# Kernel optimization log

Hardware: AMD Instinct MI355X
Metric: run time of the kernel (lower is better)

## Reference

```python
import jax, jax.numpy as jnp
import numpy as np
from math import ceil, log2

N_ROWS, M_COLS = 4096, 4096
LEVELS, FILT_LEN = 8, 16


def circ_conv(a, b, n):
    # circular convolution of each row of a with filter b, both zero-padded/truncated to length n
    return jnp.fft.irfft(jnp.fft.rfft(a, n=n) * jnp.fft.rfft(b, n=n), n=n)


def forward_level(x, w):
    # one forward DWT step over rows of x using wavelet filter w
    part = x.shape[1] // 2
    g = jnp.flip(w).at[1::2].multiply(-1.0)  # scaling filter g_k = (-1)^k h_{M-k-1}
    we, wo = w[::2], w[1::2]
    ge, go = g[::2], g[1::2]
    even, odd = x[:, ::2], x[:, 1::2]
    details = circ_conv(even, we, part) + circ_conv(odd, wo, part)
    approx = circ_conv(even, ge, part) + circ_conv(odd, go, part)
    return details, approx


def backward_level(details, approx, w):
    # one inverse DWT step: zero-upsample then circular-convolve with synthesis filters
    ws = jnp.flip(w)                       # wavelet synthesis
    ss = w.at[1::2].multiply(-1.0)         # scaling synthesis
    n, md = details.shape
    fd = jnp.zeros((n, 2 * md), details.dtype).at[:, ::2].set(details)
    fa = jnp.zeros((n, 2 * approx.shape[1]), approx.dtype).at[:, ::2].set(approx)
    return circ_conv(fd, ws, 2 * md) + circ_conv(fa, ss, 2 * approx.shape[1])


def despawn(x, wavelet):
    input_length = x.shape[1]
    target = 2 ** ceil(log2(input_length))
    x = jnp.pad(x, ((0, 0), (0, target - input_length)), mode='edge')  # ReplicationPad1d
    levels = wavelet.shape[0]
    approx = x
    coeffs = []
    for lvl in range(levels):
        d, approx = forward_level(approx, wavelet[lvl])
        coeffs.append(d)
    coeffs.append(approx)
    # inverse transform (note: original applies no thresholding in forward)
    rec = coeffs[-1]
    for lvl in reversed(range(levels)):
        rec = backward_level(coeffs[lvl], rec, wavelet[lvl])
    return rec[:, :input_length], jnp.concatenate(coeffs, axis=-1)


def setup_inputs() -> dict:
    key = jax.random.key(0)
    k1, k2 = jax.random.split(key)
    inp = jax.random.normal(k1, (N_ROWS, M_COLS), dtype=jnp.float32)
    wavelet = jax.random.normal(k2, (LEVELS, FILT_LEN), dtype=jnp.float32) * 0.3
    return {"input": inp, "wavelet": wavelet}


def reference(input, wavelet):
    return despawn(input, wavelet)
```

## Files before the change

kernel.cpp:

```cpp
#include <hip/hip_runtime.h>

#define NROWS 4096
#define NCOLS 4096
#define TPB   256

__global__ __launch_bounds__(TPB, 4) void despawn_kernel(
    const float* __restrict__ in, const float* __restrict__ wv,
    float* __restrict__ out_rec, float* __restrict__ out_coef)
{
    __shared__ float S[10240];
    float* C = S + 6144;
    const int row = blockIdx.x;
    const int tid = threadIdx.x;
    const float* rowIn = in + (size_t)row * NCOLS;

    {
        float* E = S;
        float* O = S + 2048;
        for (int i = tid; i < 1024; i += TPB) {
            float4 v = reinterpret_cast<const float4*>(rowIn)[i];
            *reinterpret_cast<float2*>(E + 2 * i) = make_float2(v.x, v.z);
            *reinterpret_cast<float2*>(O + 2 * i) = make_float2(v.y, v.w);
        }
    }
    __syncthreads();

    {
        float* E  = S;
        float* O  = S + 2048;
        float* E2 = S + 4096;
        float* O2 = S + 5120;
        int part = 2048;
        for (int lvl = 0; lvl < 8; ++lvl) {
            const float* w = wv + lvl * 16;
            float wl[16];
            #pragma unroll
            for (int q = 0; q < 16; ++q) wl[q] = w[q];
            float* det = C + (4096 - 2 * part);
            float* lastA = C + 4080;
            const bool last = (lvl == 7);
            const int pm = part - 1;
            for (int k = tid; k < part; k += TPB) {
                float d = 0.f, a = 0.f;
                #pragma unroll
                for (int t = 0; t < 8; ++t) {
                    int i = (k - t) & pm;
                    float xe = E[i], xo = O[i];
                    d = fmaf(wl[2 * t], xe, d);
                    d = fmaf(wl[2 * t + 1], xo, d);
                    a = fmaf(wl[15 - 2 * t], xe, a);
                    a = fmaf(-wl[14 - 2 * t], xo, a);
                }
                det[k] = d;
                if (last) {
                    lastA[k] = a;
                } else {
                    float* dst = (k & 1) ? O2 : E2;
                    dst[k >> 1] = a;
                }
            }
            __syncthreads();
            float* t0 = E; E = E2; E2 = t0;
            float* t1 = O; O = O2; O2 = t1;
            part >>= 1;
        }
    }

    {
        float* R0 = S;
        float* R1 = S + 4096;
        const float* A = C + 4080;
        int md = 16;
        for (int lvl = 7; lvl >= 0; --lvl) {
            const float* w = wv + lvl * 16;
            float wl[16];
            #pragma unroll
            for (int q = 0; q < 16; ++q) wl[q] = w[q];
            const float* D = C + (4096 - 2 * md);
            float* out = (lvl & 1) ? R1 : R0;
            const int mm = md - 1;
            for (int j = tid; j < md; j += TPB) {
                float r0 = 0.f, r1 = 0.f;
                #pragma unroll
                for (int t = 0; t < 8; ++t) {
                    int i = (j - t) & mm;
                    float dv = D[i], av = A[i];
                    r0 = fmaf(wl[15 - 2 * t], dv, r0);
                    r0 = fmaf(wl[2 * t],      av, r0);
                    r1 = fmaf(wl[14 - 2 * t], dv, r1);
                    r1 = fmaf(-wl[2 * t + 1], av, r1);
                }
                *reinterpret_cast<float2*>(out + 2 * j) = make_float2(r0, r1);
            }
            __syncthreads();
            A = out;
            md <<= 1;
        }
    }

    {
        const float* R0 = S;
        float* orow = out_rec  + (size_t)row * NCOLS;
        float* crow = out_coef + (size_t)row * NCOLS;
        for (int i = tid; i < 1024; i += TPB) {
            reinterpret_cast<float4*>(orow)[i] = reinterpret_cast<const float4*>(R0)[i];
            reinterpret_cast<float4*>(crow)[i] = reinterpret_cast<const float4*>(C)[i];
        }
    }
}

extern "C" void kernel_launch(void* const* d_in, const int* in_sizes, int n_in,
                              void* d_out, int out_size, void* d_ws, size_t ws_size,
                              hipStream_t stream) {
    (void)in_sizes; (void)n_in; (void)d_ws; (void)ws_size; (void)out_size;
    const float* in = (const float*)d_in[0];
    const float* wv = (const float*)d_in[1];
    float* out_rec  = (float*)d_out;
    float* out_coef = (float*)d_out + (size_t)NROWS * NCOLS;
    despawn_kernel<<<NROWS, TPB, 0, stream>>>(in, wv, out_rec, out_coef);
}
```

Before: 65.14 us.

## Register-block the large DWT levels with vectorized sliding-window LDS loads

The large forward and inverse levels now give each thread a contiguous run of 8, 4 or 2 outputs. Each thread loads a sliding window of inputs into registers with float4/float2 LDS reads, so the scalar reads of 8 taps per output go away, and it writes results with vector stores. Small levels keep one output per thread. The filter weights are now read straight from global memory through a pointer instead of being copied to a local array, and register pressure rises under the 4-blocks-per-CU launch bound.

Result: faster. 59.42 us (-8.8%).

```diff
diff --git a/kernel.cpp b/kernel.cpp
--- a/kernel.cpp
+++ b/kernel.cpp
@@ -3,6 +3,211 @@
 #define NROWS 4096
 #define NCOLS 4096
 #define TPB   256
+
+
+template<int P>
+__device__ __forceinline__ void fwd_big(const float* __restrict__ E, const float* __restrict__ O,
+                                        float* __restrict__ det, float* __restrict__ E2,
+                                        float* __restrict__ O2, const float* __restrict__ wl,
+                                        int tid)
+{
+    const int part = P * TPB;
+    const int pm4  = part / 4 - 1;
+    const int k0   = tid * P;
+    float xe[P + 8], xo[P + 8];
+    const float4* E4 = (const float4*)E;
+    const float4* O4 = (const float4*)O;
+    const int b = ((k0 - 8) >> 2) & pm4;
+    #pragma unroll
+    for (int j = 0; j < P / 4 + 2; ++j) {
+        int idx = (b + j) & pm4;
+        float4 v = E4[idx];
+        float4 u = O4[idx];
+        xe[4*j+0] = v.x; xe[4*j+1] = v.y; xe[4*j+2] = v.z; xe[4*j+3] = v.w;
+        xo[4*j+0] = u.x; xo[4*j+1] = u.y; xo[4*j+2] = u.z; xo[4*j+3] = u.w;
+    }
+    float d[P], a[P];
+    #pragma unroll
+    for (int p = 0; p < P; ++p) {
+        float dd = 0.f, aa = 0.f;
+        #pragma unroll
+        for (int t = 0; t < 8; ++t) {
+            float e = xe[p - t + 8], o = xo[p - t + 8];
+            dd = fmaf(wl[2*t],      e, dd);
+            dd = fmaf(wl[2*t+1],    o, dd);
+            aa = fmaf(wl[15-2*t],   e, aa);
+            aa = fmaf(-wl[14-2*t],  o, aa);
+        }
+        d[p] = dd; a[p] = aa;
+    }
+    #pragma unroll
+    for (int j = 0; j < P / 4; ++j)
+        ((float4*)(det + k0))[j] = make_float4(d[4*j], d[4*j+1], d[4*j+2], d[4*j+3]);
+    if (P == 8) {
+        ((float4*)(E2 + k0/2))[0] = make_float4(a[0], a[2], a[4], a[6]);
+        ((float4*)(O2 + k0/2))[0] = make_float4(a[1], a[3], a[5], a[7]);
+    } else {
+        ((float2*)(E2 + k0/2))[0] = make_float2(a[0], a[2]);
+        ((float2*)(O2 + k0/2))[0] = make_float2(a[1], a[3]);
+    }
+}
+
+__device__ __forceinline__ void fwd_mid(const float* __restrict__ E, const float* __restrict__ O,
+                                        float* __restrict__ det, float* __restrict__ E2,
+                                        float* __restrict__ O2, const float* __restrict__ wl,
+                                        int tid)
+{
+    const int pm2 = 255;
+    const int k0  = tid * 2;
+    float xe[10], xo[10];
+    const float2* Ev = (const float2*)E;
+    const float2* Ov = (const float2*)O;
+    const int b = ((k0 - 8) >> 1) & pm2;
+    #pragma unroll
+    for (int j = 0; j < 5; ++j) {
+        int idx = (b + j) & pm2;
+        float2 v = Ev[idx], u = Ov[idx];
+        xe[2*j] = v.x; xe[2*j+1] = v.y;
+        xo[2*j] = u.x; xo[2*j+1] = u.y;
+    }
+    float d[2], a[2];
+    #pragma unroll
+    for (int p = 0; p < 2; ++p) {
+        float dd = 0.f, aa = 0.f;
+        #pragma unroll
+        for (int t = 0; t < 8; ++t) {
+            float e = xe[p - t + 8], o = xo[p - t + 8];
+            dd = fmaf(wl[2*t],     e, dd);
+            dd = fmaf(wl[2*t+1],   o, dd);
+            aa = fmaf(wl[15-2*t],  e, aa);
+            aa = fmaf(-wl[14-2*t], o, aa);
+        }
+        d[p] = dd; a[p] = aa;
+    }
+    ((float2*)(det + k0))[0] = make_float2(d[0], d[1]);
+    E2[k0 >> 1] = a[0];
+    O2[k0 >> 1] = a[1];
+}
+
+__device__ __forceinline__ void fwd_small(const float* __restrict__ E, const float* __restrict__ O,
+                                          float* __restrict__ det, float* __restrict__ E2,
+                                          float* __restrict__ O2, float* __restrict__ lastA,
+                                          bool last, const float* __restrict__ wl,
+                                          int tid, int part)
+{
+    const int pm = part - 1;
+    if (tid < part) {
+        const int k = tid;
+        float dd = 0.f, aa = 0.f;
+        #pragma unroll
+        for (int t = 0; t < 8; ++t) {
+            int i = (k - t) & pm;
+            float e = E[i], o = O[i];
+            dd = fmaf(wl[2*t],     e, dd);
+            dd = fmaf(wl[2*t+1],   o, dd);
+            aa = fmaf(wl[15-2*t],  e, aa);
+            aa = fmaf(-wl[14-2*t], o, aa);
+        }
+        det[k] = dd;
+        if (last) lastA[k] = aa;
+        else { if (k & 1) O2[k >> 1] = aa; else E2[k >> 1] = aa; }
+    }
+}
+
+
+template<int P>
+__device__ __forceinline__ void bwd_big(const float* __restrict__ D, const float* __restrict__ A,
+                                        float* __restrict__ out, const float* __restrict__ wl,
+                                        int tid)
+{
+    const int md  = P * TPB;
+    const int pm4 = md / 4 - 1;
+    const int j0  = tid * P;
+    float xd[P + 8], xa[P + 8];
+    const float4* D4 = (const float4*)D;
+    const float4* A4 = (const float4*)A;
+    const int b = ((j0 - 8) >> 2) & pm4;
+    #pragma unroll
+    for (int j = 0; j < P / 4 + 2; ++j) {
+        int idx = (b + j) & pm4;
+        float4 v = D4[idx];
+        float4 u = A4[idx];
+        xd[4*j+0] = v.x; xd[4*j+1] = v.y; xd[4*j+2] = v.z; xd[4*j+3] = v.w;
+        xa[4*j+0] = u.x; xa[4*j+1] = u.y; xa[4*j+2] = u.z; xa[4*j+3] = u.w;
+    }
+    float r0[P], r1[P];
+    #pragma unroll
+    for (int p = 0; p < P; ++p) {
+        float a0 = 0.f, a1 = 0.f;
+        #pragma unroll
+        for (int t = 0; t < 8; ++t) {
+            float dv = xd[p - t + 8], av = xa[p - t + 8];
+            a0 = fmaf(wl[15-2*t],  dv, a0);
+            a0 = fmaf(wl[2*t],     av, a0);
+            a1 = fmaf(wl[14-2*t],  dv, a1);
+            a1 = fmaf(-wl[2*t+1],  av, a1);
+        }
+        r0[p] = a0; r1[p] = a1;
+    }
+    #pragma unroll
+    for (int j = 0; j < P / 2; ++j)
+        ((float4*)(out + 2*j0))[j] = make_float4(r0[2*j], r1[2*j], r0[2*j+1], r1[2*j+1]);
+}
+
+__device__ __forceinline__ void bwd_mid(const float* __restrict__ D, const float* __restrict__ A,
+                                        float* __restrict__ out, const float* __restrict__ wl,
+                                        int tid)
+{
+    const int pm2 = 255;
+    const int j0  = tid * 2;
+    float xd[10], xa[10];
+    const float2* Dv = (const float2*)D;
+    const float2* Av = (const float2*)A;
+    const int b = ((j0 - 8) >> 1) & pm2;
+    #pragma unroll
+    for (int j = 0; j < 5; ++j) {
+        int idx = (b + j) & pm2;
+        float2 v = Dv[idx], u = Av[idx];
+        xd[2*j] = v.x; xd[2*j+1] = v.y;
+        xa[2*j] = u.x; xa[2*j+1] = u.y;
+    }
+    float r0[2], r1[2];
+    #pragma unroll
+    for (int p = 0; p < 2; ++p) {
+        float a0 = 0.f, a1 = 0.f;
+        #pragma unroll
+        for (int t = 0; t < 8; ++t) {
+            float dv = xd[p - t + 8], av = xa[p - t + 8];
+            a0 = fmaf(wl[15-2*t],  dv, a0);
+            a0 = fmaf(wl[2*t],     av, a0);
+            a1 = fmaf(wl[14-2*t],  dv, a1);
+            a1 = fmaf(-wl[2*t+1],  av, a1);
+        }
+        r0[p] = a0; r1[p] = a1;
+    }
+    ((float4*)(out + 2*j0))[0] = make_float4(r0[0], r1[0], r0[1], r1[1]);
+}
+
+__device__ __forceinline__ void bwd_small(const float* __restrict__ D, const float* __restrict__ A,
+                                          float* __restrict__ out, const float* __restrict__ wl,
+                                          int tid, int md)
+{
+    const int mm = md - 1;
+    if (tid < md) {
+        const int j = tid;
+        float a0 = 0.f, a1 = 0.f;
+        #pragma unroll
+        for (int t = 0; t < 8; ++t) {
+            int i = (j - t) & mm;
+            float dv = D[i], av = A[i];
+            a0 = fmaf(wl[15-2*t],  dv, a0);
+            a0 = fmaf(wl[2*t],     av, a0);
+            a1 = fmaf(wl[14-2*t],  dv, a1);
+            a1 = fmaf(-wl[2*t+1],  av, a1);
+        }
+        ((float2*)(out + 2*j))[0] = make_float2(a0, a1);
+    }
+}
 
 __global__ __launch_bounds__(TPB, 4) void despawn_kernel(
     const float* __restrict__ in, const float* __restrict__ wv,
@@ -30,39 +235,18 @@
         float* O  = S + 2048;
         float* E2 = S + 4096;
         float* O2 = S + 5120;
-        int part = 2048;
-        for (int lvl = 0; lvl < 8; ++lvl) {
-            const float* w = wv + lvl * 16;
-            float wl[16];
-            #pragma unroll
-            for (int q = 0; q < 16; ++q) wl[q] = w[q];
-            float* det = C + (4096 - 2 * part);
-            float* lastA = C + 4080;
-            const bool last = (lvl == 7);
-            const int pm = part - 1;
-            for (int k = tid; k < part; k += TPB) {
-                float d = 0.f, a = 0.f;
-                #pragma unroll
-                for (int t = 0; t < 8; ++t) {
-                    int i = (k - t) & pm;
-                    float xe = E[i], xo = O[i];
-                    d = fmaf(wl[2 * t], xe, d);
-                    d = fmaf(wl[2 * t + 1], xo, d);
-                    a = fmaf(wl[15 - 2 * t], xe, a);
-                    a = fmaf(-wl[14 - 2 * t], xo, a);
-                }
-                det[k] = d;
-                if (last) {
-                    lastA[k] = a;
-                } else {
-                    float* dst = (k & 1) ? O2 : E2;
-                    dst[k >> 1] = a;
-                }
-            }
-            __syncthreads();
-            float* t0 = E; E = E2; E2 = t0;
-            float* t1 = O; O = O2; O2 = t1;
-            part >>= 1;
+        float* t;
+        fwd_big<8>(E, O, C + 0, E2, O2, wv + 0, tid);
+        __syncthreads(); t=E; E=E2; E2=t; t=O; O=O2; O2=t;
+        fwd_big<4>(E, O, C + 2048, E2, O2, wv + 16, tid);
+        __syncthreads(); t=E; E=E2; E2=t; t=O; O=O2; O2=t;
+        fwd_mid(E, O, C + 3072, E2, O2, wv + 32, tid);
+        __syncthreads(); t=E; E=E2; E2=t; t=O; O=O2; O2=t;
+        int part = 256;
+        for (int lvl = 3; lvl < 8; ++lvl, part >>= 1) {
+            fwd_small(E, O, C + (4096 - 2 * part), E2, O2, C + 4080,
+                      lvl == 7, wv + 16 * lvl, tid, part);
+            __syncthreads(); t=E; E=E2; E2=t; t=O; O=O2; O2=t;
         }
     }
 
@@ -71,31 +255,18 @@
         float* R1 = S + 4096;
         const float* A = C + 4080;
         int md = 16;
-        for (int lvl = 7; lvl >= 0; --lvl) {
-            const float* w = wv + lvl * 16;
-            float wl[16];
-            #pragma unroll
-            for (int q = 0; q < 16; ++q) wl[q] = w[q];
-            const float* D = C + (4096 - 2 * md);
+        for (int lvl = 7; lvl >= 3; --lvl, md <<= 1) {
             float* out = (lvl & 1) ? R1 : R0;
-            const int mm = md - 1;
-            for (int j = tid; j < md; j += TPB) {
-                float r0 = 0.f, r1 = 0.f;
-                #pragma unroll
-                for (int t = 0; t < 8; ++t) {
-                    int i = (j - t) & mm;
-                    float dv = D[i], av = A[i];
-                    r0 = fmaf(wl[15 - 2 * t], dv, r0);
-                    r0 = fmaf(wl[2 * t],      av, r0);
-                    r1 = fmaf(wl[14 - 2 * t], dv, r1);
-                    r1 = fmaf(-wl[2 * t + 1], av, r1);
-                }
-                *reinterpret_cast<float2*>(out + 2 * j) = make_float2(r0, r1);
-            }
+            bwd_small(C + (4096 - 2 * md), A, out, wv + 16 * lvl, tid, md);
             __syncthreads();
             A = out;
-            md <<= 1;
-        }
+        }
+        bwd_mid(C + 3072, A, R0, wv + 32, tid);
+        __syncthreads(); A = R0;
+        bwd_big<4>(C + 2048, A, R1, wv + 16, tid);
+        __syncthreads(); A = R1;
+        bwd_big<8>(C + 0, A, R0, wv + 0, tid);
+        __syncthreads();
     }
 
     {
```

## Register-tile wavelet levels, stream coefficients to global, shrink shared memory

Applied to the files above, without the earlier changes.

Level 0 now reads the input row directly from global memory into registers, and each thread computes several outputs from a register window instead of re-reading shared memory per tap. Large detail coefficients are written straight to the output and re-read from global memory during reconstruction, so shared memory drops to about 14KB and occupancy can rise (launch bounds go from 4 to 6). The trade-off is redundant overlapping global loads of halo data and global re-reads of detail coefficients, which may hit L2, plus more register pressure.

Result: faster. 52.41 us (-19.5%).

```diff
diff --git a/kernel.cpp b/kernel.cpp
--- a/kernel.cpp
+++ b/kernel.cpp
@@ -4,108 +4,326 @@
 #define NCOLS 4096
 #define TPB   256
 
-__global__ __launch_bounds__(TPB, 4) void despawn_kernel(
+
+__global__ __launch_bounds__(TPB, 6) void despawn_kernel(
     const float* __restrict__ in, const float* __restrict__ wv,
     float* __restrict__ out_rec, float* __restrict__ out_coef)
 {
-    __shared__ float S[10240];
-    float* C = S + 6144;
+    __shared__ float P0[2048];
+    __shared__ float P1[1024];
+    __shared__ float Csm[512];
+
+    const int tid = threadIdx.x;
     const int row = blockIdx.x;
-    const int tid = threadIdx.x;
     const float* rowIn = in + (size_t)row * NCOLS;
-
-    {
-        float* E = S;
-        float* O = S + 2048;
-        for (int i = tid; i < 1024; i += TPB) {
-            float4 v = reinterpret_cast<const float4*>(rowIn)[i];
-            *reinterpret_cast<float2*>(E + 2 * i) = make_float2(v.x, v.z);
-            *reinterpret_cast<float2*>(O + 2 * i) = make_float2(v.y, v.w);
-        }
-    }
-    __syncthreads();
-
-    {
-        float* E  = S;
-        float* O  = S + 2048;
-        float* E2 = S + 4096;
-        float* O2 = S + 5120;
-        int part = 2048;
-        for (int lvl = 0; lvl < 8; ++lvl) {
-            const float* w = wv + lvl * 16;
-            float wl[16];
-            #pragma unroll
-            for (int q = 0; q < 16; ++q) wl[q] = w[q];
-            float* det = C + (4096 - 2 * part);
-            float* lastA = C + 4080;
-            const bool last = (lvl == 7);
-            const int pm = part - 1;
-            for (int k = tid; k < part; k += TPB) {
-                float d = 0.f, a = 0.f;
+    float* crow = out_coef + (size_t)row * NCOLS;
+    float* rrow = out_rec  + (size_t)row * NCOLS;
+
+    float wl[16];
+
+    {
+        #pragma unroll
+        for (int q = 0; q < 16; ++q) wl[q] = wv[q];
+        float xw[32];
+        const float4* X4 = (const float4*)rowIn;
+        #pragma unroll
+        for (int j = 0; j < 8; ++j) {
+            int q = (4 * tid - 4 + j) & 1023;
+            float4 v = X4[q];
+            xw[4*j+0]=v.x; xw[4*j+1]=v.y; xw[4*j+2]=v.z; xw[4*j+3]=v.w;
+        }
+        float d[8], a[8];
+        #pragma unroll
+        for (int p = 0; p < 8; ++p) {
+            float dd = 0.f, aa = 0.f;
+            #pragma unroll
+            for (int t = 0; t < 8; ++t) {
+                float e = xw[16 + 2*p - 2*t];
+                float o = xw[17 + 2*p - 2*t];
+                dd = fmaf(wl[2*t],     e, dd);
+                dd = fmaf(wl[2*t+1],   o, dd);
+                aa = fmaf(wl[15-2*t],  e, aa);
+                aa = fmaf(-wl[14-2*t], o, aa);
+            }
+            d[p] = dd; a[p] = aa;
+        }
+        const int k0 = tid * 8;
+        ((float4*)(crow + k0))[0] = make_float4(d[0],d[1],d[2],d[3]);
+        ((float4*)(crow + k0))[1] = make_float4(d[4],d[5],d[6],d[7]);
+        *(float4*)(P0 + (k0>>1))        = make_float4(a[0],a[2],a[4],a[6]);
+        *(float4*)(P0 + 1024 + (k0>>1)) = make_float4(a[1],a[3],a[5],a[7]);
+    }
+    __syncthreads();
+
+    {
+        #pragma unroll
+        for (int q = 0; q < 16; ++q) wl[q] = wv[16 + q];
+        const float4* E4 = (const float4*)P0;
+        const float4* O4 = (const float4*)(P0 + 1024);
+        float xe[12], xo[12];
+        #pragma unroll
+        for (int j = 0; j < 3; ++j) {
+            int idx = (tid - 2 + j) & 255;
+            float4 v = E4[idx], u = O4[idx];
+            xe[4*j]=v.x; xe[4*j+1]=v.y; xe[4*j+2]=v.z; xe[4*j+3]=v.w;
+            xo[4*j]=u.x; xo[4*j+1]=u.y; xo[4*j+2]=u.z; xo[4*j+3]=u.w;
+        }
+        float d[4], a[4];
+        #pragma unroll
+        for (int p = 0; p < 4; ++p) {
+            float dd = 0.f, aa = 0.f;
+            #pragma unroll
+            for (int t = 0; t < 8; ++t) {
+                float e = xe[8+p-t], o = xo[8+p-t];
+                dd = fmaf(wl[2*t],     e, dd);
+                dd = fmaf(wl[2*t+1],   o, dd);
+                aa = fmaf(wl[15-2*t],  e, aa);
+                aa = fmaf(-wl[14-2*t], o, aa);
+            }
+            d[p] = dd; a[p] = aa;
+        }
+        const int k0 = tid * 4;
+        *(float4*)(crow + 2048 + k0) = make_float4(d[0],d[1],d[2],d[3]);
+        *(float2*)(P1 + (k0>>1))       = make_float2(a[0], a[2]);
+        *(float2*)(P1 + 512 + (k0>>1)) = make_float2(a[1], a[3]);
+    }
+    __syncthreads();
+
+    {
+        #pragma unroll
+        for (int q = 0; q < 16; ++q) wl[q] = wv[32 + q];
+        const float2* Ev = (const float2*)P1;
+        const float2* Ov = (const float2*)(P1 + 512);
+        float xe[10], xo[10];
+        #pragma unroll
+        for (int j = 0; j < 5; ++j) {
+            int idx = (tid - 4 + j) & 255;
+            float2 v = Ev[idx], u = Ov[idx];
+            xe[2*j]=v.x; xe[2*j+1]=v.y;
+            xo[2*j]=u.x; xo[2*j+1]=u.y;
+        }
+        float d[2], a[2];
+        #pragma unroll
+        for (int p = 0; p < 2; ++p) {
+            float dd = 0.f, aa = 0.f;
+            #pragma unroll
+            for (int t = 0; t < 8; ++t) {
+                float e = xe[8+p-t], o = xo[8+p-t];
+                dd = fmaf(wl[2*t],     e, dd);
+                dd = fmaf(wl[2*t+1],   o, dd);
+                aa = fmaf(wl[15-2*t],  e, aa);
+                aa = fmaf(-wl[14-2*t], o, aa);
+            }
+            d[p] = dd; a[p] = aa;
+        }
+        const int k0 = tid * 2;
+        *(float2*)(crow + 3072 + k0) = make_float2(d[0], d[1]);
+        P0[tid]       = a[0];
+        P0[256 + tid] = a[1];
+    }
+    __syncthreads();
+
+    {
+        float* bin  = P0;
+        float* bout = P1;
+        int part = 256;
+        int coff = 3584;
+        for (int lvl = 3; lvl < 8; ++lvl) {
+            #pragma unroll
+            for (int q = 0; q < 16; ++q) wl[q] = wv[16*lvl + q];
+            const int nth = part >> 2;
+            if (tid < nth) {
+                const int pm = nth - 1;
+                const float4* E4 = (const float4*)bin;
+                const float4* O4 = (const float4*)(bin + part);
+                float xe[12], xo[12];
                 #pragma unroll
-                for (int t = 0; t < 8; ++t) {
-                    int i = (k - t) & pm;
-                    float xe = E[i], xo = O[i];
-                    d = fmaf(wl[2 * t], xe, d);
-                    d = fmaf(wl[2 * t + 1], xo, d);
-                    a = fmaf(wl[15 - 2 * t], xe, a);
-                    a = fmaf(-wl[14 - 2 * t], xo, a);
-                }
-                det[k] = d;
-                if (last) {
-                    lastA[k] = a;
+                for (int j = 0; j < 3; ++j) {
+                    int idx = (tid - 2 + j) & pm;
+                    float4 v = E4[idx], u = O4[idx];
+                    xe[4*j]=v.x; xe[4*j+1]=v.y; xe[4*j+2]=v.z; xe[4*j+3]=v.w;
+                    xo[4*j]=u.x; xo[4*j+1]=u.y; xo[4*j+2]=u.z; xo[4*j+3]=u.w;
+                }
+                float d[4], a[4];
+                #pragma unroll
+                for (int p = 0; p < 4; ++p) {
+                    float dd = 0.f, aa = 0.f;
+                    #pragma unroll
+                    for (int t = 0; t < 8; ++t) {
+                        float e = xe[8+p-t], o = xo[8+p-t];
+                        dd = fmaf(wl[2*t],     e, dd);
+                        dd = fmaf(wl[2*t+1],   o, dd);
+                        aa = fmaf(wl[15-2*t],  e, aa);
+                        aa = fmaf(-wl[14-2*t], o, aa);
+                    }
+                    d[p] = dd; a[p] = aa;
+                }
+                const int k0 = tid * 4;
+                float4 dv = make_float4(d[0],d[1],d[2],d[3]);
+                *(float4*)(crow + coff + k0)        = dv;
+                *(float4*)(Csm + (coff - 3584) + k0) = dv;
+                if (lvl == 7) {
+                    float4 av = make_float4(a[0],a[1],a[2],a[3]);
+                    *(float4*)(crow + 4080 + k0) = av;
+                    *(float4*)(Csm + 496 + k0)   = av;
                 } else {
-                    float* dst = (k & 1) ? O2 : E2;
-                    dst[k >> 1] = a;
+                    *(float2*)(bout + (k0>>1))              = make_float2(a[0], a[2]);
+                    *(float2*)(bout + (part>>1) + (k0>>1))  = make_float2(a[1], a[3]);
                 }
             }
             __syncthreads();
-            float* t0 = E; E = E2; E2 = t0;
-            float* t1 = O; O = O2; O2 = t1;
+            float* tmp = bin; bin = bout; bout = tmp;
+            coff += part;
             part >>= 1;
         }
     }
 
-    {
-        float* R0 = S;
-        float* R1 = S + 4096;
-        const float* A = C + 4080;
+    const float* A = Csm + 496;
+    {
+        float* bo   = P0;
+        float* balt = P1;
         int md = 16;
-        for (int lvl = 7; lvl >= 0; --lvl) {
-            const float* w = wv + lvl * 16;
-            float wl[16];
-            #pragma unroll
-            for (int q = 0; q < 16; ++q) wl[q] = w[q];
-            const float* D = C + (4096 - 2 * md);
-            float* out = (lvl & 1) ? R1 : R0;
-            const int mm = md - 1;
-            for (int j = tid; j < md; j += TPB) {
-                float r0 = 0.f, r1 = 0.f;
+        int doffL = 480;
+        for (int lvl = 7; lvl >= 3; --lvl) {
+            #pragma unroll
+            for (int q = 0; q < 16; ++q) wl[q] = wv[16*lvl + q];
+            const int nth = md >> 2;
+            if (tid < nth) {
+                const int pm = nth - 1;
+                const float4* D4 = (const float4*)(Csm + doffL);
+                const float4* A4 = (const float4*)A;
+                float xd[12], xa[12];
                 #pragma unroll
-                for (int t = 0; t < 8; ++t) {
-                    int i = (j - t) & mm;
-                    float dv = D[i], av = A[i];
-                    r0 = fmaf(wl[15 - 2 * t], dv, r0);
-                    r0 = fmaf(wl[2 * t],      av, r0);
-                    r1 = fmaf(wl[14 - 2 * t], dv, r1);
-                    r1 = fmaf(-wl[2 * t + 1], av, r1);
-                }
-                *reinterpret_cast<float2*>(out + 2 * j) = make_float2(r0, r1);
+                for (int j = 0; j < 3; ++j) {
+                    int idx = (tid - 2 + j) & pm;
+                    float4 v = D4[idx], u = A4[idx];
+                    xd[4*j]=v.x; xd[4*j+1]=v.y; xd[4*j+2]=v.z; xd[4*j+3]=v.w;
+                    xa[4*j]=u.x; xa[4*j+1]=u.y; xa[4*j+2]=u.z; xa[4*j+3]=u.w;
+                }
+                float r0[4], r1[4];
+                #pragma unroll
+                for (int p = 0; p < 4; ++p) {
+                    float a0 = 0.f, a1 = 0.f;
+                    #pragma unroll
+                    for (int t = 0; t < 8; ++t) {
+                        float dv = xd[8+p-t], av = xa[8+p-t];
+                        a0 = fmaf(wl[15-2*t], dv, a0);
+                        a0 = fmaf(wl[2*t],    av, a0);
+                        a1 = fmaf(wl[14-2*t], dv, a1);
+                        a1 = fmaf(-wl[2*t+1], av, a1);
+                    }
+                    r0[p] = a0; r1[p] = a1;
+                }
+                const int j0 = tid * 4;
+                ((float4*)(bo + 2*j0))[0] = make_float4(r0[0],r1[0],r0[1],r1[1]);
+                ((float4*)(bo + 2*j0))[1] = make_float4(r0[2],r1[2],r0[3],r1[3]);
             }
             __syncthreads();
-            A = out;
+            A = bo;
+            float* tmp = bo; bo = balt; balt = tmp;
             md <<= 1;
-        }
-    }
-
-    {
-        const float* R0 = S;
-        float* orow = out_rec  + (size_t)row * NCOLS;
-        float* crow = out_coef + (size_t)row * NCOLS;
-        for (int i = tid; i < 1024; i += TPB) {
-            reinterpret_cast<float4*>(orow)[i] = reinterpret_cast<const float4*>(R0)[i];
-            reinterpret_cast<float4*>(crow)[i] = reinterpret_cast<const float4*>(C)[i];
-        }
+            doffL -= md;
+        }
+    }
+
+    {
+        #pragma unroll
+        for (int q = 0; q < 16; ++q) wl[q] = wv[32 + q];
+        const float2* Dg = (const float2*)(crow + 3072);
+        const float2* A2 = (const float2*)A;
+        float xd[10], xa[10];
+        #pragma unroll
+        for (int j = 0; j < 5; ++j) {
+            int idx = (tid - 4 + j) & 255;
+            float2 v = Dg[idx], u = A2[idx];
+            xd[2*j]=v.x; xd[2*j+1]=v.y;
+            xa[2*j]=u.x; xa[2*j+1]=u.y;
+        }
+        float r0[2], r1[2];
+        #pragma unroll
+        for (int p = 0; p < 2; ++p) {
+            float a0 = 0.f, a1 = 0.f;
+            #pragma unroll
+            for (int t = 0; t < 8; ++t) {
+                float dv = xd[8+p-t], av = xa[8+p-t];
+                a0 = fmaf(wl[15-2*t], dv, a0);
+                a0 = fmaf(wl[2*t],    av, a0);
+                a1 = fmaf(wl[14-2*t], dv, a1);
+                a1 = fmaf(-wl[2*t+1], av, a1);
+            }
+            r0[p] = a0; r1[p] = a1;
+        }
+        const int j0 = tid * 2;
+        *(float4*)(P1 + 2*j0) = make_float4(r0[0],r1[0],r0[1],r1[1]);
+    }
+    __syncthreads();
+
+    {
+        #pragma unroll
+        for (int q = 0; q < 16; ++q) wl[q] = wv[16 + q];
+        const float4* Dg = (const float4*)(crow + 2048);
+        const float4* A4 = (const float4*)P1;
+        float xd[12], xa[12];
+        #pragma unroll
+        for (int j = 0; j < 3; ++j) {
+            int idx = (tid - 2 + j) & 255;
+            float4 v = Dg[idx], u = A4[idx];
+            xd[4*j]=v.x; xd[4*j+1]=v.y; xd[4*j+2]=v.z; xd[4*j+3]=v.w;
+            xa[4*j]=u.x; xa[4*j+1]=u.y; xa[4*j+2]=u.z; xa[4*j+3]=u.w;
+        }
+        float r0[4], r1[4];
+        #pragma unroll
+        for (int p = 0; p < 4; ++p) {
+            float a0 = 0.f, a1 = 0.f;
+            #pragma unroll
+            for (int t = 0; t < 8; ++t) {
+                float dv = xd[8+p-t], av = xa[8+p-t];
+                a0 = fmaf(wl[15-2*t], dv, a0);
+                a0 = fmaf(wl[2*t],    av, a0);
+                a1 = fmaf(wl[14-2*t], dv, a1);
+                a1 = fmaf(-wl[2*t+1], av, a1);
+            }
+            r0[p] = a0; r1[p] = a1;
+        }
+        const int j0 = tid * 4;
+        ((float4*)(P0 + 2*j0))[0] = make_float4(r0[0],r1[0],r0[1],r1[1]);
+        ((float4*)(P0 + 2*j0))[1] = make_float4(r0[2],r1[2],r0[3],r1[3]);
+    }
+    __syncthreads();
+
+    {
+        #pragma unroll
+        for (int q = 0; q < 16; ++q) wl[q] = wv[q];
+        const float4* Dg = (const float4*)crow;
+        const float4* A4 = (const float4*)P0;
+        float xd[16], xa[16];
+        #pragma unroll
+        for (int j = 0; j < 4; ++j) {
+            int idx = (2*tid - 2 + j) & 511;
+            float4 v = Dg[idx], u = A4[idx];
+            xd[4*j]=v.x; xd[4*j+1]=v.y; xd[4*j+2]=v.z; xd[4*j+3]=v.w;
+            xa[4*j]=u.x; xa[4*j+1]=u.y; xa[4*j+2]=u.z; xa[4*j+3]=u.w;
+        }
+        float r0[8], r1[8];
+        #pragma unroll
+        for (int p = 0; p < 8; ++p) {
+            float a0 = 0.f, a1 = 0.f;
+            #pragma unroll
+            for (int t = 0; t < 8; ++t) {
+                float dv = xd[8+p-t], av = xa[8+p-t];
+                a0 = fmaf(wl[15-2*t], dv, a0);
+                a0 = fmaf(wl[2*t],    av, a0);
+                a1 = fmaf(wl[14-2*t], dv, a1);
+                a1 = fmaf(-wl[2*t+1], av, a1);
+            }
+            r0[p] = a0; r1[p] = a1;
+        }
+        const int j0 = tid * 8;
+        float4* R = (float4*)(rrow + 2*j0);
+        R[0] = make_float4(r0[0],r1[0],r0[1],r1[1]);
+        R[1] = make_float4(r0[2],r1[2],r0[3],r1[3]);
+        R[2] = make_float4(r0[4],r1[4],r0[5],r1[5]);
+        R[3] = make_float4(r0[6],r1[6],r0[7],r1[7]);
     }
 }
 
```
